# Performance work log

Measured on AMD Instinct MI355X. Metric: run time of the kernel, lower is better.

Reference implementation:

```python
import jax, jax.numpy as jnp
import numpy as np

ATT_SIZE = 32
HEAD_NUM = 2


def setup_inputs() -> dict:
    key = jax.random.key(0)
    k_in, k_q, k_k, k_v, k_r = jax.random.split(key, 5)
    B, F, D = 16384, 32, 64
    H = ATT_SIZE * HEAD_NUM  # 64
    inputs = jax.random.normal(k_in, (B, F, D), dtype=jnp.float32)
    W_Query = jax.random.truncated_normal(k_q, -2.0, 2.0, (D, H), dtype=jnp.float32) * 0.05
    W_Key = jax.random.truncated_normal(k_k, -2.0, 2.0, (D, H), dtype=jnp.float32) * 0.05
    W_Value = jax.random.truncated_normal(k_v, -2.0, 2.0, (D, H), dtype=jnp.float32) * 0.05
    W_Res = jax.random.truncated_normal(k_r, -2.0, 2.0, (D, H), dtype=jnp.float32) * 0.05
    return {"inputs": inputs, "W_Query": W_Query, "W_Key": W_Key, "W_Value": W_Value, "W_Res": W_Res}


def reference(inputs, W_Query, W_Key, W_Value, W_Res):
    B, F, D = inputs.shape
    h, a = HEAD_NUM, ATT_SIZE
    # project and reshape to [B, h, F, a]
    q = jnp.einsum('bfd,de->bfe', inputs, W_Query).reshape(B, F, h, a).transpose(0, 2, 1, 3)
    k = jnp.einsum('bfd,de->bfe', inputs, W_Key).reshape(B, F, h, a).transpose(0, 2, 1, 3)
    v = jnp.einsum('bfd,de->bfe', inputs, W_Value).reshape(B, F, h, a).transpose(0, 2, 1, 3)
    # NOTE: original code has NO 1/sqrt(d) scaling
    scores = jnp.einsum('bhqa,bhka->bhqk', q, k)
    attn = jax.nn.softmax(scores, axis=-1)
    out = jnp.einsum('bhqk,bhka->bhqa', attn, v)  # [B, h, F, a]
    out = out.transpose(0, 2, 1, 3).reshape(B, F, h * a)
    out = out + jnp.einsum('bfd,de->bfe', inputs, W_Res)
    return jax.nn.relu(out)
```

## Files before the change

kernel.cpp:

```cpp
#include <hip/hip_runtime.h>


constexpr int kF = 32, kD = 64, kH = 64;

constexpr int XS = 72;
constexpr int QS = 72;
constexpr int VS = 40;
constexpr int PS = 40;

using short8  = __attribute__((ext_vector_type(8))) short;
using float4v = __attribute__((ext_vector_type(4))) float;

__device__ __forceinline__ unsigned short f2bf(float x) {
    unsigned u = __float_as_uint(x);
    u += 0x7FFF + ((u >> 16) & 1);
    return (unsigned short)(u >> 16);
}
__device__ __forceinline__ float bf2f(unsigned short b) {
    return __uint_as_float((unsigned)b << 16);
}

__global__ void wprep_kernel(const float* __restrict__ Wq, const float* __restrict__ Wk,
                             const float* __restrict__ Wv, const float* __restrict__ Wr,
                             unsigned short* __restrict__ wt) {
    const int m = blockIdx.x;
    const float* __restrict__ W = (m == 0) ? Wq : (m == 1) ? Wk : (m == 2) ? Wv : Wr;
    for (int i = threadIdx.x; i < kD * kH; i += blockDim.x) {
        const int e = i >> 6, d = i & 63;
        wt[m * kD * kH + e * kD + d] = f2bf(W[d * kH + e]);
    }
}

__global__ __launch_bounds__(256)
void interact_mfma(const float* __restrict__ X, const unsigned short* __restrict__ Wt,
                   float* __restrict__ out)
{
    __shared__ __align__(16) unsigned short s_x [kF * XS];
    __shared__ __align__(16) unsigned short s_q [kF * QS];
    __shared__ __align__(16) unsigned short s_k [kF * QS];
    __shared__ __align__(16) unsigned short s_r [kF * QS];
    __shared__ __align__(16) unsigned short s_vt[kH * VS];
    __shared__ __align__(16) unsigned short s_p [2 * kF * PS];

    const int t    = threadIdx.x;
    const int w    = t >> 6;
    const int lane = t & 63;
    const int quad = lane >> 4;
    const int l    = lane & 15;
    const int b    = blockIdx.x;

    short8 bfrag[4][2];
    {
        const unsigned short* __restrict__ wtm = Wt + w * (kD * kH);
        #pragma unroll
        for (int nt = 0; nt < 4; ++nt)
            #pragma unroll
            for (int ks = 0; ks < 2; ++ks)
                bfrag[nt][ks] =
                    *reinterpret_cast<const short8*>(wtm + (16 * nt + l) * kD + 32 * ks + quad * 8);
    }

    const float* __restrict__ Xb = X + (size_t)b * (kF * kD);
    #pragma unroll
    for (int i = 0; i < 2; ++i) {
        const int idx = i * 256 + t;
        const int f = idx >> 4, c = idx & 15;
        const float4 v = reinterpret_cast<const float4*>(Xb)[idx];
        ushort4 pk;
        pk.x = f2bf(v.x); pk.y = f2bf(v.y); pk.z = f2bf(v.z); pk.w = f2bf(v.w);
        *reinterpret_cast<ushort4*>(&s_x[f * XS + c * 4]) = pk;
    }
    __syncthreads();

    {
        float4v acc[2][4];
        #pragma unroll
        for (int mt = 0; mt < 2; ++mt)
            #pragma unroll
            for (int nt = 0; nt < 4; ++nt)
                acc[mt][nt] = (float4v){0.f, 0.f, 0.f, 0.f};

        short8 afrag[2][2];
        #pragma unroll
        for (int mt = 0; mt < 2; ++mt)
            #pragma unroll
            for (int ks = 0; ks < 2; ++ks)
                afrag[mt][ks] =
                    *reinterpret_cast<const short8*>(&s_x[(16 * mt + l) * XS + 32 * ks + quad * 8]);

        #pragma unroll
        for (int mt = 0; mt < 2; ++mt)
            #pragma unroll
            for (int nt = 0; nt < 4; ++nt) {
                acc[mt][nt] = __builtin_amdgcn_mfma_f32_16x16x32_bf16(
                    afrag[mt][0], bfrag[nt][0], acc[mt][nt], 0, 0, 0);
                acc[mt][nt] = __builtin_amdgcn_mfma_f32_16x16x32_bf16(
                    afrag[mt][1], bfrag[nt][1], acc[mt][nt], 0, 0, 0);
            }

        if (w == 2) {
            #pragma unroll
            for (int mt = 0; mt < 2; ++mt)
                #pragma unroll
                for (int nt = 0; nt < 4; ++nt)
                    #pragma unroll
                    for (int r = 0; r < 4; ++r)
                        s_vt[(16 * nt + l) * VS + 16 * mt + quad * 4 + r] = f2bf(acc[mt][nt][r]);
        } else {
            unsigned short* __restrict__ dst = (w == 0) ? s_q : (w == 1) ? s_k : s_r;
            #pragma unroll
            for (int mt = 0; mt < 2; ++mt)
                #pragma unroll
                for (int nt = 0; nt < 4; ++nt)
                    #pragma unroll
                    for (int r = 0; r < 4; ++r)
                        dst[(16 * mt + quad * 4 + r) * QS + 16 * nt + l] = f2bf(acc[mt][nt][r]);
        }
    }
    __syncthreads();

    const int h  = w >> 1;
    const int mt = w & 1;
    float inv[4];
    {
        const short8 qa =
            *reinterpret_cast<const short8*>(&s_q[(16 * mt + l) * QS + 32 * h + quad * 8]);
        const short8 kb0 =
            *reinterpret_cast<const short8*>(&s_k[(l) * QS + 32 * h + quad * 8]);
        const short8 kb1 =
            *reinterpret_cast<const short8*>(&s_k[(16 + l) * QS + 32 * h + quad * 8]);

        float4v s0 = (float4v){0.f, 0.f, 0.f, 0.f};
        float4v s1 = (float4v){0.f, 0.f, 0.f, 0.f};
        s0 = __builtin_amdgcn_mfma_f32_16x16x32_bf16(qa, kb0, s0, 0, 0, 0);
        s1 = __builtin_amdgcn_mfma_f32_16x16x32_bf16(qa, kb1, s1, 0, 0, 0);

        #pragma unroll
        for (int r = 0; r < 4; ++r) {
            float m = fmaxf(s0[r], s1[r]);
            #pragma unroll
            for (int d = 1; d < 16; d <<= 1) m = fmaxf(m, __shfl_xor(m, d));
            const float e0 = __expf(s0[r] - m);
            const float e1 = __expf(s1[r] - m);
            float sum = e0 + e1;
            #pragma unroll
            for (int d = 1; d < 16; d <<= 1) sum += __shfl_xor(sum, d);
            inv[r] = 1.0f / sum;
            const int row = 16 * mt + quad * 4 + r;
            s_p[(h * kF + row) * PS + l]      = f2bf(e0);
            s_p[(h * kF + row) * PS + 16 + l] = f2bf(e1);
        }
    }
    __syncthreads();

    {
        const short8 pa =
            *reinterpret_cast<const short8*>(&s_p[(h * kF + 16 * mt + l) * PS + quad * 8]);
        const short8 vb0 =
            *reinterpret_cast<const short8*>(&s_vt[(32 * h + l) * VS + quad * 8]);
        const short8 vb1 =
            *reinterpret_cast<const short8*>(&s_vt[(32 * h + 16 + l) * VS + quad * 8]);

        float4v o0 = (float4v){0.f, 0.f, 0.f, 0.f};
        float4v o1 = (float4v){0.f, 0.f, 0.f, 0.f};
        o0 = __builtin_amdgcn_mfma_f32_16x16x32_bf16(pa, vb0, o0, 0, 0, 0);
        o1 = __builtin_amdgcn_mfma_f32_16x16x32_bf16(pa, vb1, o1, 0, 0, 0);

        float* __restrict__ Ob = out + (size_t)b * (kF * kH);
        #pragma unroll
        for (int r = 0; r < 4; ++r) {
            const int f = 16 * mt + quad * 4 + r;
            const float rv0 = bf2f(s_r[f * QS + 32 * h + l]);
            const float rv1 = bf2f(s_r[f * QS + 32 * h + 16 + l]);
            Ob[f * kH + 32 * h + l]      = fmaxf(o0[r] * inv[r] + rv0, 0.0f);
            Ob[f * kH + 32 * h + 16 + l] = fmaxf(o1[r] * inv[r] + rv1, 0.0f);
        }
    }
}

extern "C" void kernel_launch(void* const* d_in, const int* in_sizes, int n_in,
                              void* d_out, int out_size, void* d_ws, size_t ws_size,
                              hipStream_t stream) {
    const float* X  = (const float*)d_in[0];
    const float* Wq = (const float*)d_in[1];
    const float* Wk = (const float*)d_in[2];
    const float* Wv = (const float*)d_in[3];
    const float* Wr = (const float*)d_in[4];
    float* out = (float*)d_out;
    unsigned short* wt = (unsigned short*)d_ws;

    wprep_kernel<<<4, 256, 0, stream>>>(Wq, Wk, Wv, Wr, wt);

    const int B = in_sizes[0] / (kF * kD);
    interact_mfma<<<B, 256, 0, stream>>>(X, wt, out);
}
```

Measured before the change: 278.9 us.

## Load X fragments directly from global and keep residual projection in registers

```diff
diff --git a/kernel.cpp b/kernel.cpp
--- a/kernel.cpp
+++ b/kernel.cpp
@@ -3,7 +3,6 @@
 
 constexpr int kF = 32, kD = 64, kH = 64;
 
-constexpr int XS = 72;
 constexpr int QS = 72;
 constexpr int VS = 40;
 constexpr int PS = 40;
@@ -11,13 +10,13 @@
 using short8  = __attribute__((ext_vector_type(8))) short;
 using float4v = __attribute__((ext_vector_type(4))) float;
 
-__device__ __forceinline__ unsigned short f2bf(float x) {
+__device__ __forceinline__ unsigned short f2bf_rne(float x) {
     unsigned u = __float_as_uint(x);
     u += 0x7FFF + ((u >> 16) & 1);
     return (unsigned short)(u >> 16);
 }
-__device__ __forceinline__ float bf2f(unsigned short b) {
-    return __uint_as_float((unsigned)b << 16);
+__device__ __forceinline__ unsigned pk_bf16(float lo, float hi) {
+    return (unsigned)f2bf_rne(lo) | ((unsigned)f2bf_rne(hi) << 16);
 }
 
 __global__ void wprep_kernel(const float* __restrict__ Wq, const float* __restrict__ Wk,
@@ -27,18 +26,16 @@
     const float* __restrict__ W = (m == 0) ? Wq : (m == 1) ? Wk : (m == 2) ? Wv : Wr;
     for (int i = threadIdx.x; i < kD * kH; i += blockDim.x) {
         const int e = i >> 6, d = i & 63;
-        wt[m * kD * kH + e * kD + d] = f2bf(W[d * kH + e]);
-    }
-}
-
-__global__ __launch_bounds__(256)
+        wt[m * kD * kH + e * kD + d] = f2bf_rne(W[d * kH + e]);
+    }
+}
+
+__global__ __launch_bounds__(256, 4)
 void interact_mfma(const float* __restrict__ X, const unsigned short* __restrict__ Wt,
                    float* __restrict__ out)
 {
-    __shared__ __align__(16) unsigned short s_x [kF * XS];
     __shared__ __align__(16) unsigned short s_q [kF * QS];
     __shared__ __align__(16) unsigned short s_k [kF * QS];
-    __shared__ __align__(16) unsigned short s_r [kF * QS];
     __shared__ __align__(16) unsigned short s_vt[kH * VS];
     __shared__ __align__(16) unsigned short s_p [2 * kF * PS];
 
@@ -49,30 +46,52 @@
     const int l    = lane & 15;
     const int b    = blockIdx.x;
 
-    short8 bfrag[4][2];
+    const int h   = w >> 1;
+    const int mtw = w & 1;
+
+    const float* __restrict__ Xb = X + (size_t)b * (kF * kD);
+
+    auto load_xa = [&](int mt, int ks) -> short8 {
+        const float* p = Xb + (16 * mt + l) * kD + 32 * ks + quad * 8;
+        const float4 a = *reinterpret_cast<const float4*>(p);
+        const float4 c = *reinterpret_cast<const float4*>(p + 4);
+        union { unsigned u[4]; short8 v; } r;
+        r.u[0] = pk_bf16(a.x, a.y);
+        r.u[1] = pk_bf16(a.z, a.w);
+        r.u[2] = pk_bf16(c.x, c.y);
+        r.u[3] = pk_bf16(c.z, c.w);
+        return r.v;
+    };
+
+    short8 xa_own[2];
+    xa_own[0] = load_xa(mtw, 0);
+    xa_own[1] = load_xa(mtw, 1);
+
+    float4v racc[2];
+    racc[0] = (float4v){0.f, 0.f, 0.f, 0.f};
+    racc[1] = (float4v){0.f, 0.f, 0.f, 0.f};
     {
+        const unsigned short* __restrict__ wtr = Wt + 3 * (kD * kH);
+        #pragma unroll
+        for (int i = 0; i < 2; ++i) {
+            const int nt = 2 * h + i;
+            #pragma unroll
+            for (int ks = 0; ks < 2; ++ks) {
+                const short8 rb = *reinterpret_cast<const short8*>(
+                    wtr + (16 * nt + l) * kD + 32 * ks + quad * 8);
+                racc[i] = __builtin_amdgcn_mfma_f32_16x16x32_bf16(xa_own[ks], rb, racc[i], 0, 0, 0);
+            }
+        }
+    }
+
+    if (w < 2) {
         const unsigned short* __restrict__ wtm = Wt + w * (kD * kH);
-        #pragma unroll
-        for (int nt = 0; nt < 4; ++nt)
-            #pragma unroll
-            for (int ks = 0; ks < 2; ++ks)
-                bfrag[nt][ks] =
-                    *reinterpret_cast<const short8*>(wtm + (16 * nt + l) * kD + 32 * ks + quad * 8);
-    }
-
-    const float* __restrict__ Xb = X + (size_t)b * (kF * kD);
-    #pragma unroll
-    for (int i = 0; i < 2; ++i) {
-        const int idx = i * 256 + t;
-        const int f = idx >> 4, c = idx & 15;
-        const float4 v = reinterpret_cast<const float4*>(Xb)[idx];
-        ushort4 pk;
-        pk.x = f2bf(v.x); pk.y = f2bf(v.y); pk.z = f2bf(v.z); pk.w = f2bf(v.w);
-        *reinterpret_cast<ushort4*>(&s_x[f * XS + c * 4]) = pk;
-    }
-    __syncthreads();
-
-    {
+        short8 xa[2][2];
+        #pragma unroll
+        for (int ks = 0; ks < 2; ++ks) xa[mtw][ks] = xa_own[ks];
+        #pragma unroll
+        for (int ks = 0; ks < 2; ++ks) xa[1 - mtw][ks] = load_xa(1 - mtw, ks);
+
         float4v acc[2][4];
         #pragma unroll
         for (int mt = 0; mt < 2; ++mt)
@@ -80,53 +99,57 @@
             for (int nt = 0; nt < 4; ++nt)
                 acc[mt][nt] = (float4v){0.f, 0.f, 0.f, 0.f};
 
-        short8 afrag[2][2];
+        #pragma unroll
+        for (int nt = 0; nt < 4; ++nt) {
+            #pragma unroll
+            for (int ks = 0; ks < 2; ++ks) {
+                const short8 bf = *reinterpret_cast<const short8*>(
+                    wtm + (16 * nt + l) * kD + 32 * ks + quad * 8);
+                #pragma unroll
+                for (int mt = 0; mt < 2; ++mt)
+                    acc[mt][nt] = __builtin_amdgcn_mfma_f32_16x16x32_bf16(xa[mt][ks], bf, acc[mt][nt], 0, 0, 0);
+            }
+        }
+
+        unsigned short* __restrict__ dst = (w == 0) ? s_q : s_k;
         #pragma unroll
         for (int mt = 0; mt < 2; ++mt)
             #pragma unroll
-            for (int ks = 0; ks < 2; ++ks)
-                afrag[mt][ks] =
-                    *reinterpret_cast<const short8*>(&s_x[(16 * mt + l) * XS + 32 * ks + quad * 8]);
-
-        #pragma unroll
-        for (int mt = 0; mt < 2; ++mt)
-            #pragma unroll
-            for (int nt = 0; nt < 4; ++nt) {
-                acc[mt][nt] = __builtin_amdgcn_mfma_f32_16x16x32_bf16(
-                    afrag[mt][0], bfrag[nt][0], acc[mt][nt], 0, 0, 0);
-                acc[mt][nt] = __builtin_amdgcn_mfma_f32_16x16x32_bf16(
-                    afrag[mt][1], bfrag[nt][1], acc[mt][nt], 0, 0, 0);
+            for (int nt = 0; nt < 4; ++nt)
+                #pragma unroll
+                for (int r = 0; r < 4; ++r)
+                    dst[(16 * mt + quad * 4 + r) * QS + 16 * nt + l] = f2bf_rne(acc[mt][nt][r]);
+    } else {
+        const unsigned short* __restrict__ wtm = Wt + 2 * (kD * kH);
+        float4v acc[4];
+        #pragma unroll
+        for (int nt = 0; nt < 4; ++nt) acc[nt] = (float4v){0.f, 0.f, 0.f, 0.f};
+
+        #pragma unroll
+        for (int nt = 0; nt < 4; ++nt)
+            #pragma unroll
+            for (int ks = 0; ks < 2; ++ks) {
+                const short8 bf = *reinterpret_cast<const short8*>(
+                    wtm + (16 * nt + l) * kD + 32 * ks + quad * 8);
+                acc[nt] = __builtin_amdgcn_mfma_f32_16x16x32_bf16(xa_own[ks], bf, acc[nt], 0, 0, 0);
             }
 
-        if (w == 2) {
-            #pragma unroll
-            for (int mt = 0; mt < 2; ++mt)
-                #pragma unroll
-                for (int nt = 0; nt < 4; ++nt)
-                    #pragma unroll
-                    for (int r = 0; r < 4; ++r)
-                        s_vt[(16 * nt + l) * VS + 16 * mt + quad * 4 + r] = f2bf(acc[mt][nt][r]);
-        } else {
-            unsigned short* __restrict__ dst = (w == 0) ? s_q : (w == 1) ? s_k : s_r;
-            #pragma unroll
-            for (int mt = 0; mt < 2; ++mt)
-                #pragma unroll
-                for (int nt = 0; nt < 4; ++nt)
-                    #pragma unroll
-                    for (int r = 0; r < 4; ++r)
-                        dst[(16 * mt + quad * 4 + r) * QS + 16 * nt + l] = f2bf(acc[mt][nt][r]);
+        #pragma unroll
+        for (int nt = 0; nt < 4; ++nt) {
+            unsigned* dst = reinterpret_cast<unsigned*>(
+                &s_vt[(16 * nt + l) * VS + 16 * mtw + quad * 4]);
+            dst[0] = pk_bf16(acc[nt][0], acc[nt][1]);
+            dst[1] = pk_bf16(acc[nt][2], acc[nt][3]);
         }
     }
     __syncthreads();
 
-    const int h  = w >> 1;
-    const int mt = w & 1;
     float inv[4];
     {
         const short8 qa =
-            *reinterpret_cast<const short8*>(&s_q[(16 * mt + l) * QS + 32 * h + quad * 8]);
+            *reinterpret_cast<const short8*>(&s_q[(16 * mtw + l) * QS + 32 * h + quad * 8]);
         const short8 kb0 =
-            *reinterpret_cast<const short8*>(&s_k[(l) * QS + 32 * h + quad * 8]);
+            *reinterpret_cast<const short8*>(&s_k[l * QS + 32 * h + quad * 8]);
         const short8 kb1 =
             *reinterpret_cast<const short8*>(&s_k[(16 + l) * QS + 32 * h + quad * 8]);
 
@@ -146,16 +169,16 @@
             #pragma unroll
             for (int d = 1; d < 16; d <<= 1) sum += __shfl_xor(sum, d);
             inv[r] = 1.0f / sum;
-            const int row = 16 * mt + quad * 4 + r;
-            s_p[(h * kF + row) * PS + l]      = f2bf(e0);
-            s_p[(h * kF + row) * PS + 16 + l] = f2bf(e1);
+            const int row = h * kF + 16 * mtw + quad * 4 + r;
+            s_p[row * PS + l]      = f2bf_rne(e0);
+            s_p[row * PS + 16 + l] = f2bf_rne(e1);
         }
     }
     __syncthreads();
 
     {
         const short8 pa =
-            *reinterpret_cast<const short8*>(&s_p[(h * kF + 16 * mt + l) * PS + quad * 8]);
+            *reinterpret_cast<const short8*>(&s_p[(h * kF + 16 * mtw + l) * PS + quad * 8]);
         const short8 vb0 =
             *reinterpret_cast<const short8*>(&s_vt[(32 * h + l) * VS + quad * 8]);
         const short8 vb1 =
@@ -169,11 +192,9 @@
         float* __restrict__ Ob = out + (size_t)b * (kF * kH);
         #pragma unroll
         for (int r = 0; r < 4; ++r) {
-            const int f = 16 * mt + quad * 4 + r;
-            const float rv0 = bf2f(s_r[f * QS + 32 * h + l]);
-            const float rv1 = bf2f(s_r[f * QS + 32 * h + 16 + l]);
-            Ob[f * kH + 32 * h + l]      = fmaxf(o0[r] * inv[r] + rv0, 0.0f);
-            Ob[f * kH + 32 * h + 16 + l] = fmaxf(o1[r] * inv[r] + rv1, 0.0f);
+            const int f = 16 * mtw + quad * 4 + r;
+            Ob[f * kH + 32 * h + l]      = fmaxf(o0[r] * inv[r] + racc[0][r], 0.0f);
+            Ob[f * kH + 32 * h + 16 + l] = fmaxf(o1[r] * inv[r] + racc[1][r], 0.0f);
         }
     }
 }
```

Result: slower. 351.8 us (+26.1%).
